# Kernel optimization log

Hardware: AMD Instinct MI355X
Metric: run time of the kernel (lower is better)

Reference implementation:

```python
import jax, jax.numpy as jnp
import numpy as np

B, D, NUM_HOP, NUM_REL = 8192, 512, 8, 2000  # batch, input_dim, num_hop, num_relation
TAU = 1.0


def setup_inputs() -> dict:
    key = jax.random.key(0)
    ks = jax.random.split(key, 7)
    s = 1.0 / np.sqrt(D)  # PyTorch GRU uniform init bound
    return {
        "query": jax.random.normal(ks[0], (B, D), jnp.float32),
        "W_ih": jax.random.uniform(ks[1], (3 * D, D), jnp.float32, -s, s),
        "W_hh": jax.random.uniform(ks[2], (3 * D, D), jnp.float32, -s, s),
        "b_ih": jax.random.uniform(ks[3], (3 * D,), jnp.float32, -s, s),
        "b_hh": jax.random.uniform(ks[4], (3 * D,), jnp.float32, -s, s),
        "relation": jax.random.normal(ks[5], (2 * NUM_REL, D), jnp.float32),
        "eos": jax.random.normal(ks[6], (1, D), jnp.float32),
    }


def gru_cell(x, h, W_ih, W_hh, b_ih, b_hh):
    # PyTorch nn.GRU cell, gate order (r, z, n)
    gi = x @ W_ih.T + b_ih  # [B, 3D]
    gh = h @ W_hh.T + b_hh  # [B, 3D]
    ir, iz, i_n = jnp.split(gi, 3, axis=-1)
    hr, hz, h_n = jnp.split(gh, 3, axis=-1)
    r = jax.nn.sigmoid(ir + hr)
    z = jax.nn.sigmoid(iz + hz)
    n = jnp.tanh(i_n + r * h_n)
    return (1.0 - z) * n + z * h


def reference(query, W_ih, W_hh, b_ih, b_hh, relation, eos):
    # gru over seq [query, eos] starting from h0 = 0; hidden[1:] == final hx for 1 layer
    h0 = jnp.zeros_like(query)
    h1 = gru_cell(query, h0, W_ih, W_hh, b_ih, b_hh)
    hidden = gru_cell(jnp.broadcast_to(eos, query.shape), h1, W_ih, W_hh, b_ih, b_hh)

    def step(h, _):
        score = jnp.einsum('bd,rd->br', h, relation)          # [B, 2R]
        attention = jax.nn.softmax(score / TAU, axis=-1)
        subgoal = jnp.einsum('br,rd->bd', attention, relation)  # [B, D]
        h_new = gru_cell(subgoal, h, W_ih, W_hh, b_ih, b_hh)
        return h_new, subgoal

    _, subgoals = jax.lax.scan(step, hidden, None, length=NUM_HOP)  # [NUM_HOP, B, D]
    subgoals = jnp.moveaxis(subgoals, 0, 1)  # [B, NUM_HOP, D]
    masks = jnp.ones(subgoals.shape[:-1], dtype=bool)
    return subgoals, masks
```

## Files before the change

### kernel.cpp

```cpp
#include <hip/hip_runtime.h>


typedef _Float16 f16;
typedef _Float16 f16x8 __attribute__((ext_vector_type(8)));
typedef _Float16 f16x4 __attribute__((ext_vector_type(4)));
typedef float    f32x4 __attribute__((ext_vector_type(4)));

constexpr int BATCH = 8192;
constexpr int DDIM  = 512;
constexpr int D3    = 1536;
constexpr int NRELT = 4000;
constexpr int NRELP = 4096;
constexpr int NHOP  = 8;

#define MFMA16(a,b,c) __builtin_amdgcn_mfma_f32_16x16x32_f16((a),(b),(c),0,0,0)
#define BAR()   __builtin_amdgcn_s_barrier()
#define FENCE() asm volatile("" ::: "memory")
#define SCHED0() __builtin_amdgcn_sched_barrier(0)
#define VM(n) asm volatile("s_waitcnt vmcnt(" #n ")" ::: "memory")

__device__ __forceinline__ void gll16(const void* g, void* l) {
  __builtin_amdgcn_global_load_lds(
      (const __attribute__((address_space(1))) unsigned int*)g,
      (__attribute__((address_space(3))) unsigned int*)l, 16, 0, 0);
}

__global__ __launch_bounds__(256) void k_split(const float* __restrict__ src,
                                               f16* __restrict__ hi, f16* __restrict__ lo, int n) {
  int i = blockIdx.x * 256 + threadIdx.x;
  if (i >= n) return;
  float v = src[i];
  f16 h = (f16)v;
  hi[i] = h;
  lo[i] = (f16)(v - (float)h);
}

__global__ __launch_bounds__(256) void k_prep_rel(const float* __restrict__ rel,
    f16* __restrict__ rhi, f16* __restrict__ rlo,
    f16* __restrict__ thi, f16* __restrict__ tlo) {
  int i = blockIdx.x * 256 + threadIdx.x;
  if (i >= NRELP * DDIM) return;
  int r = i >> 9, d = i & 511;
  float v = (r < NRELT) ? rel[i] : 0.f;
  f16 h = (f16)v, l = (f16)(v - (float)h);
  rhi[i] = h; rlo[i] = l;
  thi[(size_t)d * NRELP + r] = h;
  tlo[(size_t)d * NRELP + r] = l;
}

__global__ __launch_bounds__(64) void k_gieos(const float* __restrict__ W,
                                              const float* __restrict__ eos,
                                              float* __restrict__ out) {
  int o = blockIdx.x;
  float s = 0.f;
  for (int i = threadIdx.x; i < DDIM; i += 64) s += W[(size_t)o * DDIM + i] * eos[i];
  for (int off = 32; off; off >>= 1) s += __shfl_xor(s, off);
  if (threadIdx.x == 0) out[o] = s;
}

template<int EPI>
__device__ __forceinline__ void gemm_core(
    const f16* __restrict__ Ahi, const f16* __restrict__ Alo, int lda,
    const f16* __restrict__ Bhi, const f16* __restrict__ Blo, int ldb,
    float* __restrict__ Cout, f16* __restrict__ Chi, f16* __restrict__ Clo,
    int ldc, int m0, int n0, int kst, int nt, f16* lds)
{
  const int tid  = threadIdx.x;
  const int lane = tid & 63;
  const int wave = tid >> 6;
  const int wm = wave >> 2;
  const int wn = wave & 3;
  const int rb = lane & 15;
  const int sl = lane >> 4;
  const int srow = lane >> 2;

  auto stage2 = [&](int buf, int p, int k0) {
    const f16* src = (p == 0) ? Ahi : (p == 1) ? Alo : (p == 2) ? Bhi : Blo;
    const int ld   = (p < 2) ? lda : ldb;
    const int base = (p < 2) ? m0 : n0;
    f16* pl = lds + ((buf * 4 + p) << 13);
    #pragma unroll
    for (int c = 0; c < 2; ++c) {
      const int r0 = wave * 16 + c * 128;
      const int lr = r0 + srow;
      const int slot = (lane & 3) ^ ((lr >> 1) & 3);
      gll16(src + (size_t)(base + lr) * ld + k0 + slot * 8, pl + r0 * 32);
    }
  };
  auto rd = [&](int buf, int p, int lr) -> f16x8 {
    const int off = lr * 64 + ((sl ^ ((lr >> 1) & 3)) << 4);
    return *(const f16x8*)((const char*)(lds + ((buf * 4 + p) << 13)) + off);
  };

  stage2(0, 0, kst); stage2(0, 2, kst); stage2(0, 1, kst); stage2(0, 3, kst);

  f32x4 acc[8][4] = {};
  f16x8 ah[8], al[8], bh[4], bl[4];
  const int A0 = wm * 128, B0 = wn * 64;

  for (int t = 0; t < nt; ++t) {
    const int cur = t & 1;
    const int nxt = cur ^ 1;
    const bool more = (t + 1 < nt);
    const int kn = kst + (t + 1) * 32;

    VM(0);
    BAR(); FENCE();
    #pragma unroll
    for (int f = 0; f < 4; ++f) bh[f] = rd(cur, 2, B0 + f * 16 + rb);
    #pragma unroll
    for (int f = 0; f < 8; ++f) ah[f] = rd(cur, 0, A0 + f * 16 + rb);
    #pragma unroll
    for (int f = 0; f < 8; ++f) al[f] = rd(cur, 1, A0 + f * 16 + rb);
    #pragma unroll
    for (int f = 0; f < 4; ++f) bl[f] = rd(cur, 3, B0 + f * 16 + rb);
    if (more) { stage2(nxt, 0, kn); stage2(nxt, 2, kn);
                stage2(nxt, 1, kn); stage2(nxt, 3, kn); }
    __builtin_amdgcn_s_setprio(1);
    #pragma unroll
    for (int m = 0; m < 8; ++m)
      #pragma unroll
      for (int n = 0; n < 4; ++n)
        acc[m][n] = MFMA16(ah[m], bh[n], acc[m][n]);
    #pragma unroll
    for (int m = 0; m < 8; ++m)
      #pragma unroll
      for (int n = 0; n < 4; ++n)
        acc[m][n] = MFMA16(al[m], bh[n], acc[m][n]);
    #pragma unroll
    for (int m = 0; m < 8; ++m)
      #pragma unroll
      for (int n = 0; n < 4; ++n)
        acc[m][n] = MFMA16(ah[m], bl[n], acc[m][n]);
    __builtin_amdgcn_s_setprio(0);
    SCHED0();
  }

  #pragma unroll
  for (int fm = 0; fm < 8; ++fm)
    #pragma unroll
    for (int fn = 0; fn < 4; ++fn)
      #pragma unroll
      for (int r = 0; r < 4; ++r) {
        const int gr = m0 + wm * 128 + fm * 16 + sl * 4 + r;
        const int gc = n0 + wn * 64 + fn * 16 + rb;
        const float v = acc[fm][fn][r];
        if constexpr (EPI == 0) {
          Cout[(size_t)gr * ldc + gc] = v;
        } else {
          const f16 vh = (f16)v;
          Chi[(size_t)gr * ldc + gc] = vh;
          Clo[(size_t)gr * ldc + gc] = (f16)(v - (float)vh);
        }
      }
}

template<int EPI>
__global__ __launch_bounds__(512, 2)
void k_gemm8(const f16* __restrict__ Ahi, const f16* __restrict__ Alo, int lda,
             const f16* __restrict__ Bhi, const f16* __restrict__ Blo, int ldb,
             float* __restrict__ Cout, f16* __restrict__ Chi, f16* __restrict__ Clo,
             int ldc, int K, int gy, int nblocks)
{
  __shared__ __align__(16) f16 lds[2 * 4 * 256 * 32];
  const int bid = blockIdx.x;
  const int id2 = (bid & 7) * (nblocks >> 3) + (bid >> 3);
  const int m = id2 & 31;
  const int rest = id2 >> 5;
  const int n = rest % gy;
  const int z = rest / gy;
  float* Co = Cout ? Cout + (size_t)z * BATCH * (size_t)ldc : nullptr;
  gemm_core<EPI>(Ahi, Alo, lda, Bhi, Blo, ldb, Co, Chi, Clo, ldc,
                 m * 256, n * 256, z * K, K / 32, lds);
}

__global__ __launch_bounds__(512, 2)
void k_gemm8_gru(const f16* __restrict__ xhi, const f16* __restrict__ xlo,
                 const f16* __restrict__ hhi, const f16* __restrict__ hlo,
                 const f16* __restrict__ wihhi, const f16* __restrict__ wihlo,
                 const f16* __restrict__ whhhi, const f16* __restrict__ whhlo,
                 float* __restrict__ gi, float* __restrict__ gh)
{
  __shared__ __align__(16) f16 lds[2 * 4 * 256 * 32];
  const int bid = blockIdx.x;
  const int id2 = (bid & 7) * 48 + (bid >> 3);
  const int m = id2 & 31;
  const int nn = id2 >> 5;
  const bool second = nn >= 6;
  gemm_core<0>(second ? hhi : xhi, second ? hlo : xlo, DDIM,
               second ? whhhi : wihhi, second ? whhlo : wihlo, DDIM,
               second ? gh : gi, nullptr, nullptr, D3,
               m * 256, (second ? nn - 6 : nn) * 256, 0, DDIM / 32, lds);
}

__global__ __launch_bounds__(256)
void k_softmax(f16* __restrict__ Shi, f16* __restrict__ Slo) {
  const int row = blockIdx.x;
  f16* phi = Shi + (size_t)row * NRELP;
  f16* plo = Slo + (size_t)row * NRELP;
  const int tid = threadIdx.x, lane = tid & 63, wv = tid >> 6;
  const int ng = (tid < 232) ? 4 : 3;
  f32x4 v[4];
  float mx = -3.402823e38f;
  #pragma unroll
  for (int i = 0; i < 4; ++i)
    if (i < ng) {
      f16x4 hv = *(const f16x4*)(phi + (tid + 256 * i) * 4);
      f16x4 lv = *(const f16x4*)(plo + (tid + 256 * i) * 4);
      #pragma unroll
      for (int j = 0; j < 4; ++j) v[i][j] = (float)hv[j] + (float)lv[j];
      mx = fmaxf(fmaxf(fmaxf(mx, v[i][0]), fmaxf(v[i][1], v[i][2])), v[i][3]);
    }
  float l = 0.f;
  #pragma unroll
  for (int i = 0; i < 4; ++i)
    if (i < ng)
      l += __expf(v[i][0] - mx) + __expf(v[i][1] - mx)
         + __expf(v[i][2] - mx) + __expf(v[i][3] - mx);
  #pragma unroll
  for (int off = 1; off < 64; off <<= 1) {
    float om = __shfl_xor(mx, off), ol = __shfl_xor(l, off);
    float nm = fmaxf(mx, om);
    l = l * __expf(mx - nm) + ol * __expf(om - nm);
    mx = nm;
  }
  __shared__ float sm[4], slr[4];
  if (lane == 0) { sm[wv] = mx; slr[wv] = l; }
  __syncthreads();
  const float fm = fmaxf(fmaxf(sm[0], sm[1]), fmaxf(sm[2], sm[3]));
  const float fl = slr[0] * __expf(sm[0] - fm) + slr[1] * __expf(sm[1] - fm)
                 + slr[2] * __expf(sm[2] - fm) + slr[3] * __expf(sm[3] - fm);
  const float il = 1.f / fl;
  #pragma unroll
  for (int i = 0; i < 4; ++i)
    if (i < ng) {
      f16x4 oh, ol;
      #pragma unroll
      for (int j = 0; j < 4; ++j) {
        const float pv = __expf(v[i][j] - fm) * il;
        const f16 ph = (f16)pv;
        oh[j] = ph;
        ol[j] = (f16)(pv - (float)ph);
      }
      *(f16x4*)(phi + (tid + 256 * i) * 4) = oh;
      *(f16x4*)(plo + (tid + 256 * i) * 4) = ol;
    }
  if (tid < 24) {
    f16x4 z = {(f16)0.f, (f16)0.f, (f16)0.f, (f16)0.f};
    *(f16x4*)(phi + (1000 + tid) * 4) = z;
    *(f16x4*)(plo + (1000 + tid) * 4) = z;
  }
}

__global__ __launch_bounds__(256)
void k_subred(const float* __restrict__ Cp, float* __restrict__ outp,
              f16* __restrict__ xhi, f16* __restrict__ xlo, int hop) {
  const int idx = blockIdx.x * 256 + threadIdx.x;
  const int b = idx >> 7, d4 = (idx & 127) * 4;
  const size_t o = (size_t)b * DDIM + d4;
  f32x4 s = *(const f32x4*)(Cp + o);
  s += *(const f32x4*)(Cp + (size_t)BATCH * DDIM + o);
  s += *(const f32x4*)(Cp + 2 * (size_t)BATCH * DDIM + o);
  s += *(const f32x4*)(Cp + 3 * (size_t)BATCH * DDIM + o);
  *(f32x4*)(outp + (size_t)b * (NHOP * DDIM) + (size_t)hop * DDIM + d4) = s;
  f16x4 vh, vl;
  #pragma unroll
  for (int j = 0; j < 4; ++j) {
    const f16 ph = (f16)s[j];
    vh[j] = ph;
    vl[j] = (f16)(s[j] - (float)ph);
  }
  *(f16x4*)(xhi + o) = vh;
  *(f16x4*)(xlo + o) = vl;
}

__global__ __launch_bounds__(256)
void k_gates(const float* __restrict__ gi, const float* __restrict__ givec,
             const float* __restrict__ gh,
             const float* __restrict__ bih, const float* __restrict__ bhh,
             const float* __restrict__ hin, float* __restrict__ hout,
             f16* __restrict__ hhi, f16* __restrict__ hlo)
{
  const int idx = blockIdx.x * 256 + threadIdx.x;
  const int b  = idx >> 7;
  const int d4 = (idx & 127) * 4;
  f32x4 ir, iz, inn;
  if (gi) {
    const float* g = gi + (size_t)b * D3 + d4;
    ir  = *(const f32x4*)(g);
    iz  = *(const f32x4*)(g + DDIM);
    inn = *(const f32x4*)(g + 2 * DDIM);
  } else {
    ir  = *(const f32x4*)(givec + d4);
    iz  = *(const f32x4*)(givec + DDIM + d4);
    inn = *(const f32x4*)(givec + 2 * DDIM + d4);
  }
  ir  += *(const f32x4*)(bih + d4);
  iz  += *(const f32x4*)(bih + DDIM + d4);
  inn += *(const f32x4*)(bih + 2 * DDIM + d4);
  f32x4 hr = {0.f, 0.f, 0.f, 0.f}, hz = {0.f, 0.f, 0.f, 0.f}, hn = {0.f, 0.f, 0.f, 0.f};
  if (gh) {
    const float* g = gh + (size_t)b * D3 + d4;
    hr = *(const f32x4*)(g);
    hz = *(const f32x4*)(g + DDIM);
    hn = *(const f32x4*)(g + 2 * DDIM);
  }
  hr += *(const f32x4*)(bhh + d4);
  hz += *(const f32x4*)(bhh + DDIM + d4);
  hn += *(const f32x4*)(bhh + 2 * DDIM + d4);
  f32x4 hp = {0.f, 0.f, 0.f, 0.f};
  if (hin) hp = *(const f32x4*)(hin + (size_t)b * DDIM + d4);
  f32x4 hv; f16x4 vh, vl;
  #pragma unroll
  for (int j = 0; j < 4; ++j) {
    const float r = 1.f / (1.f + __expf(-(ir[j] + hr[j])));
    const float z = 1.f / (1.f + __expf(-(iz[j] + hz[j])));
    const float n = tanhf(inn[j] + r * hn[j]);
    const float h = (1.f - z) * n + z * hp[j];
    hv[j] = h;
    const f16 ph = (f16)h;
    vh[j] = ph;
    vl[j] = (f16)(h - (float)ph);
  }
  *(f32x4*)(hout + (size_t)b * DDIM + d4) = hv;
  *(f16x4*)(hhi + (size_t)b * DDIM + d4) = vh;
  *(f16x4*)(hlo + (size_t)b * DDIM + d4) = vl;
}

__global__ __launch_bounds__(256) void k_ones(float* __restrict__ o, int n) {
  int i = blockIdx.x * 256 + threadIdx.x;
  if (i < n) o[i] = 1.0f;
}

extern "C" void kernel_launch(void* const* d_in, const int* in_sizes, int n_in,
                              void* d_out, int out_size, void* d_ws, size_t ws_size,
                              hipStream_t stream)
{
  const float* query = (const float*)d_in[0];
  const float* W_ih  = (const float*)d_in[1];
  const float* W_hh  = (const float*)d_in[2];
  const float* b_ih  = (const float*)d_in[3];
  const float* b_hh  = (const float*)d_in[4];
  const float* rel   = (const float*)d_in[5];
  const float* eos   = (const float*)d_in[6];
  float* out = (float*)d_out;
  (void)in_sizes; (void)n_in; (void)out_size; (void)ws_size;

  char* w = (char*)d_ws;
  f16* SPhi    = (f16*)w;   w += (size_t)BATCH * NRELP * 2;
  f16* SPlo    = (f16*)w;   w += (size_t)BATCH * NRELP * 2;
  float* Cpart = (float*)w; w += (size_t)4 * BATCH * DDIM * 4;
  float* hbuf  = (float*)w; w += (size_t)BATCH * DDIM * 4;
  f16* h_hi    = (f16*)w;   w += (size_t)BATCH * DDIM * 2;
  f16* h_lo    = (f16*)w;   w += (size_t)BATCH * DDIM * 2;
  f16* x_hi    = (f16*)w;   w += (size_t)BATCH * DDIM * 2;
  f16* x_lo    = (f16*)w;   w += (size_t)BATCH * DDIM * 2;
  f16* wih_hi  = (f16*)w;   w += (size_t)D3 * DDIM * 2;
  f16* wih_lo  = (f16*)w;   w += (size_t)D3 * DDIM * 2;
  f16* whh_hi  = (f16*)w;   w += (size_t)D3 * DDIM * 2;
  f16* whh_lo  = (f16*)w;   w += (size_t)D3 * DDIM * 2;
  f16* rel_hi  = (f16*)w;   w += (size_t)NRELP * DDIM * 2;
  f16* rel_lo  = (f16*)w;   w += (size_t)NRELP * DDIM * 2;
  f16* relT_hi = (f16*)w;   w += (size_t)DDIM * NRELP * 2;
  f16* relT_lo = (f16*)w;   w += (size_t)DDIM * NRELP * 2;
  float* gieos = (float*)w; w += (size_t)D3 * 4;
  float* gi = (float*)SPhi;
  float* gh = (float*)SPhi + (size_t)BATCH * D3;

  k_split<<<(BATCH * DDIM + 255) / 256, 256, 0, stream>>>(query, x_hi, x_lo, BATCH * DDIM);
  k_split<<<(D3 * DDIM + 255) / 256, 256, 0, stream>>>(W_ih, wih_hi, wih_lo, D3 * DDIM);
  k_split<<<(D3 * DDIM + 255) / 256, 256, 0, stream>>>(W_hh, whh_hi, whh_lo, D3 * DDIM);
  k_prep_rel<<<(NRELP * DDIM + 255) / 256, 256, 0, stream>>>(rel, rel_hi, rel_lo, relT_hi, relT_lo);
  k_gieos<<<D3, 64, 0, stream>>>(W_ih, eos, gieos);

  const int ggrid = BATCH * DDIM / 4 / 256;

  k_gemm8<0><<<192, 512, 0, stream>>>(x_hi, x_lo, DDIM, wih_hi, wih_lo, DDIM,
      gi, nullptr, nullptr, D3, DDIM, 6, 192);
  k_gates<<<ggrid, 256, 0, stream>>>(gi, nullptr, nullptr, b_ih, b_hh, nullptr, hbuf, h_hi, h_lo);

  k_gemm8<0><<<192, 512, 0, stream>>>(h_hi, h_lo, DDIM, whh_hi, whh_lo, DDIM,
      gh, nullptr, nullptr, D3, DDIM, 6, 192);
  k_gates<<<ggrid, 256, 0, stream>>>(nullptr, gieos, gh, b_ih, b_hh, hbuf, hbuf, h_hi, h_lo);

  for (int hop = 0; hop < NHOP; ++hop) {
    k_gemm8<1><<<512, 512, 0, stream>>>(h_hi, h_lo, DDIM, rel_hi, rel_lo, DDIM,
        nullptr, SPhi, SPlo, NRELP, DDIM, 16, 512);
    k_softmax<<<BATCH, 256, 0, stream>>>(SPhi, SPlo);
    k_gemm8<0><<<256, 512, 0, stream>>>(SPhi, SPlo, NRELP,
        relT_hi, relT_lo, NRELP, Cpart, nullptr, nullptr, DDIM, 1024, 2, 256);
    k_subred<<<ggrid, 256, 0, stream>>>(Cpart, out, x_hi, x_lo, hop);
    k_gemm8_gru<<<384, 512, 0, stream>>>(x_hi, x_lo, h_hi, h_lo,
        wih_hi, wih_lo, whh_hi, whh_lo, gi, gh);
    k_gates<<<ggrid, 256, 0, stream>>>(gi, nullptr, gh, b_ih, b_hh, hbuf, hbuf, h_hi, h_lo);
  }

  k_ones<<<(BATCH * NHOP + 255) / 256, 256, 0, stream>>>(out + (size_t)BATCH * NHOP * DDIM, BATCH * NHOP);
}
```

Baseline: 3.087 ms.

## Interleave LDS reads, prefetch stages and MFMA blocks in split-f16 GEMM loop

The GEMM main loop is restructured into six phases. Each phase reads a quarter of the A/B fragments from LDS, issues one of the next tile's global-to-LDS stages, then runs a 4x4 MFMA block, with barriers between phases. The wait at the top of the loop now allows two outstanding loads instead of draining the queue, and the al register array is halved to cut register pressure. The aim is to overlap global loads and LDS reads with MFMA work, in exchange for many extra workgroup barriers per iteration.

```diff
diff --git a/kernel.cpp b/kernel.cpp
--- a/kernel.cpp
+++ b/kernel.cpp
@@ -18,6 +18,7 @@
 #define FENCE() asm volatile("" ::: "memory")
 #define SCHED0() __builtin_amdgcn_sched_barrier(0)
 #define VM(n) asm volatile("s_waitcnt vmcnt(" #n ")" ::: "memory")
+#define LGKM0() asm volatile("s_waitcnt lgkmcnt(0)" ::: "memory")
 
 __device__ __forceinline__ void gll16(const void* g, void* l) {
   __builtin_amdgcn_global_load_lds(
@@ -95,7 +96,7 @@
   stage2(0, 0, kst); stage2(0, 2, kst); stage2(0, 1, kst); stage2(0, 3, kst);
 
   f32x4 acc[8][4] = {};
-  f16x8 ah[8], al[8], bh[4], bl[4];
+  f16x8 ah[8], al[4], bh[4], bl[4];
   const int A0 = wm * 128, B0 = wn * 64;
 
   for (int t = 0; t < nt; ++t) {
@@ -104,36 +105,86 @@
     const bool more = (t + 1 < nt);
     const int kn = kst + (t + 1) * 32;
 
-    VM(0);
+    if (more) { stage2(nxt, 0, kn); VM(2); } else { VM(0); }
     BAR(); FENCE();
     #pragma unroll
     for (int f = 0; f < 4; ++f) bh[f] = rd(cur, 2, B0 + f * 16 + rb);
     #pragma unroll
-    for (int f = 0; f < 8; ++f) ah[f] = rd(cur, 0, A0 + f * 16 + rb);
-    #pragma unroll
-    for (int f = 0; f < 8; ++f) al[f] = rd(cur, 1, A0 + f * 16 + rb);
+    for (int f = 0; f < 4; ++f) ah[f] = rd(cur, 0, A0 + f * 16 + rb);
+    LGKM0(); SCHED0();
+    __builtin_amdgcn_s_setprio(1);
+    #pragma unroll
+    for (int m = 0; m < 4; ++m)
+      #pragma unroll
+      for (int n = 0; n < 4; ++n)
+        acc[m][n] = MFMA16(ah[m], bh[n], acc[m][n]);
+    __builtin_amdgcn_s_setprio(0);
+    FENCE(); BAR();
+
+    #pragma unroll
+    for (int f = 0; f < 4; ++f) ah[4 + f] = rd(cur, 0, A0 + 64 + f * 16 + rb);
+    if (more) stage2(nxt, 2, kn);
+    FENCE(); BAR(); FENCE();
+    LGKM0(); SCHED0();
+    __builtin_amdgcn_s_setprio(1);
+    #pragma unroll
+    for (int m = 0; m < 4; ++m)
+      #pragma unroll
+      for (int n = 0; n < 4; ++n)
+        acc[4 + m][n] = MFMA16(ah[4 + m], bh[n], acc[4 + m][n]);
+    __builtin_amdgcn_s_setprio(0);
+    FENCE(); BAR();
+
     #pragma unroll
     for (int f = 0; f < 4; ++f) bl[f] = rd(cur, 3, B0 + f * 16 + rb);
-    if (more) { stage2(nxt, 0, kn); stage2(nxt, 2, kn);
-                stage2(nxt, 1, kn); stage2(nxt, 3, kn); }
-    __builtin_amdgcn_s_setprio(1);
-    #pragma unroll
-    for (int m = 0; m < 8; ++m)
-      #pragma unroll
-      for (int n = 0; n < 4; ++n)
-        acc[m][n] = MFMA16(ah[m], bh[n], acc[m][n]);
-    #pragma unroll
-    for (int m = 0; m < 8; ++m)
+    if (more) stage2(nxt, 1, kn);
+    FENCE(); BAR(); FENCE();
+    LGKM0(); SCHED0();
+    __builtin_amdgcn_s_setprio(1);
+    #pragma unroll
+    for (int m = 0; m < 4; ++m)
+      #pragma unroll
+      for (int n = 0; n < 4; ++n)
+        acc[m][n] = MFMA16(ah[m], bl[n], acc[m][n]);
+    __builtin_amdgcn_s_setprio(0);
+    FENCE(); BAR();
+
+    if (more) stage2(nxt, 3, kn);
+    FENCE(); BAR(); FENCE();
+    __builtin_amdgcn_s_setprio(1);
+    #pragma unroll
+    for (int m = 0; m < 4; ++m)
+      #pragma unroll
+      for (int n = 0; n < 4; ++n)
+        acc[4 + m][n] = MFMA16(ah[4 + m], bl[n], acc[4 + m][n]);
+    __builtin_amdgcn_s_setprio(0);
+    FENCE(); BAR();
+
+    #pragma unroll
+    for (int f = 0; f < 4; ++f) al[f] = rd(cur, 1, A0 + f * 16 + rb);
+    FENCE(); BAR(); FENCE();
+    LGKM0(); SCHED0();
+    __builtin_amdgcn_s_setprio(1);
+    #pragma unroll
+    for (int m = 0; m < 4; ++m)
       #pragma unroll
       for (int n = 0; n < 4; ++n)
         acc[m][n] = MFMA16(al[m], bh[n], acc[m][n]);
-    #pragma unroll
-    for (int m = 0; m < 8; ++m)
-      #pragma unroll
-      for (int n = 0; n < 4; ++n)
-        acc[m][n] = MFMA16(ah[m], bl[n], acc[m][n]);
-    __builtin_amdgcn_s_setprio(0);
-    SCHED0();
+    __builtin_amdgcn_s_setprio(0);
+    FENCE(); BAR();
+
+    #pragma unroll
+    for (int f = 0; f < 4; ++f) al[f] = rd(cur, 1, A0 + 64 + f * 16 + rb);
+    FENCE(); BAR(); FENCE();
+    LGKM0(); SCHED0();
+    __builtin_amdgcn_s_setprio(1);
+    #pragma unroll
+    for (int m = 0; m < 4; ++m)
+      #pragma unroll
+      for (int n = 0; n < 4; ++n)
+        acc[4 + m][n] = MFMA16(al[m], bh[n], acc[4 + m][n]);
+    __builtin_amdgcn_s_setprio(0);
+    FENCE(); BAR();
   }
 
   #pragma unroll
```

After: 3.196 ms. +3.5%, slower.
